# Optimization experiments

Measured on AMD Instinct MI355X. Metric: run time of the kernel, lower is better.

The kernel has to match this reference:

```python
import jax, jax.numpy as jnp
import numpy as np

N_NODES = 50000
N_EDGES = 800000
HIDDEN = 128
NUM_LAYERS = 3
NEG_SLOPE = 0.2  # PyG GATConv default leaky_relu slope


def setup_inputs() -> dict:
    key = jax.random.key(0)
    ks = jax.random.split(key, 10)
    d = HIDDEN
    glorot = 1.0 / np.sqrt(d)
    inp = {
        "x": jax.random.normal(ks[0], (N_NODES, d), dtype=jnp.float32),
        "edge_index": jax.random.randint(ks[1], (2, N_EDGES), 0, N_NODES, dtype=jnp.int32),
        "edge_mask": jax.random.uniform(ks[2], (N_EDGES,), dtype=jnp.float32),
        # GATConv params (heads=1)
        "W_gat": jax.random.normal(ks[3], (d, d), dtype=jnp.float32) * glorot,
        "a_src": jax.random.normal(ks[4], (d,), dtype=jnp.float32) * glorot,
        "a_dst": jax.random.normal(ks[5], (d,), dtype=jnp.float32) * glorot,
        "b_gat": jnp.zeros((d,), dtype=jnp.float32),
        # Stacked GCNConv params
        "W_gcn": jax.random.normal(ks[6], (NUM_LAYERS, d, d), dtype=jnp.float32) * glorot,
        "b_gcn": jnp.zeros((NUM_LAYERS, d), dtype=jnp.float32),
    }
    return inp


def _seg_softmax(e, seg, n):
    m = jax.ops.segment_max(e, seg, num_segments=n)
    p = jnp.exp(e - m[seg])
    s = jax.ops.segment_sum(p, seg, num_segments=n)
    return p / s[seg]


def reference(x, edge_index, edge_mask, W_gat, a_src, a_dst, b_gat, W_gcn, b_gcn):
    N = x.shape[0]
    loops = jnp.arange(N, dtype=edge_index.dtype)
    src = jnp.concatenate([edge_index[0], loops])  # [E+N] with self loops
    dst = jnp.concatenate([edge_index[1], loops])

    # --- GATConv (heads=1, add_self_loops=True); edge_attr ignored (edge_dim=None) ---
    xp = x @ W_gat                                      # [N, d]
    e = jax.nn.leaky_relu((xp @ a_src)[src] + (xp @ a_dst)[dst], NEG_SLOPE)
    alpha = _seg_softmax(e, dst, N)                     # segment softmax over incoming edges
    h = jax.ops.segment_sum(alpha[:, None] * xp[src], dst, num_segments=N) + b_gat

    # --- GCN normalization with edge_mask as edge_weight (self-loop weight = 1) ---
    w = jnp.concatenate([edge_mask, jnp.ones((N,), dtype=edge_mask.dtype)])
    deg = jax.ops.segment_sum(w, dst, num_segments=N)
    dinv = jnp.where(deg > 0, jax.lax.rsqrt(jnp.maximum(deg, 1e-12)), 0.0)
    norm = dinv[src] * w * dinv[dst]                    # [E+N]

    outs = [h]
    for l in range(NUM_LAYERS):
        z = outs[-1] @ W_gcn[l]                         # [N, d]
        z = jax.ops.segment_sum(norm[:, None] * z[src], dst, num_segments=N) + b_gcn[l]
        outs.append(jax.nn.relu(z))

    # JumpingKnowledge 'max': elementwise max over layer outputs
    return jnp.max(jnp.stack(outs, axis=0), axis=0)
```

## Files before the change

kernel.cpp:

```cpp
#include <hip/hip_runtime.h>

#define HIDDEN 128
#define NEG_SLOPE 0.2f
#define P_SORT 256

typedef unsigned short ushort_t;
typedef __attribute__((ext_vector_type(8))) short short8;
typedef __attribute__((ext_vector_type(4))) float floatx4;

static inline size_t align_up(size_t x, size_t a){ return (x + a - 1) & ~(a - 1); }

__device__ __forceinline__ ushort_t f2b(float f){
  unsigned u = __float_as_uint(f);
  unsigned r = (u + 0x7FFFu + ((u >> 16) & 1u)) >> 16;
  return (ushort_t)r;
}

__device__ __forceinline__ float b2f(ushort_t u){
  return __uint_as_float(((unsigned)u) << 16);
}

__device__ __forceinline__ void fma8q(float* acc, uint2 v, float a){
  int x = (int)v.x, y = (int)v.y;
  acc[0] += a * (float)((x << 24) >> 24);
  acc[1] += a * (float)((x << 16) >> 24);
  acc[2] += a * (float)((x <<  8) >> 24);
  acc[3] += a * (float)( x        >> 24);
  acc[4] += a * (float)((y << 24) >> 24);
  acc[5] += a * (float)((y << 16) >> 24);
  acc[6] += a * (float)((y <<  8) >> 24);
  acc[7] += a * (float)( y        >> 24);
}

__device__ __forceinline__ uint2 packq8(const float* f, float qi){
  unsigned a = 0, b = 0;
  int q;
  q = (int)rintf(f[0]*qi); a |= ((unsigned)q & 255u);
  q = (int)rintf(f[1]*qi); a |= ((unsigned)q & 255u) << 8;
  q = (int)rintf(f[2]*qi); a |= ((unsigned)q & 255u) << 16;
  q = (int)rintf(f[3]*qi); a |= ((unsigned)q & 255u) << 24;
  q = (int)rintf(f[4]*qi); b |= ((unsigned)q & 255u);
  q = (int)rintf(f[5]*qi); b |= ((unsigned)q & 255u) << 8;
  q = (int)rintf(f[6]*qi); b |= ((unsigned)q & 255u) << 16;
  q = (int)rintf(f[7]*qi); b |= ((unsigned)q & 255u) << 24;
  uint2 r; r.x = a; r.y = b; return r;
}

__device__ __forceinline__ uint4 pack8(const float* f){
  uint4 u;
  u.x = (unsigned)f2b(f[0]) | ((unsigned)f2b(f[1]) << 16);
  u.y = (unsigned)f2b(f[2]) | ((unsigned)f2b(f[3]) << 16);
  u.z = (unsigned)f2b(f[4]) | ((unsigned)f2b(f[5]) << 16);
  u.w = (unsigned)f2b(f[6]) | ((unsigned)f2b(f[7]) << 16);
  return u;
}


__global__ __launch_bounds__(256) void k_b1cnt_cast(const int* __restrict__ dst,
                                                    int* __restrict__ bcnt,
                                                    const float* __restrict__ Wg,
                                                    const float* __restrict__ Wc,
                                                    ushort_t* __restrict__ Wt,
                                                    int E, int epb, int nbkt){
  int t = threadIdx.x;
  if (blockIdx.x >= P_SORT){
    int i = (blockIdx.x - P_SORT)*256 + t;
    int mat = i >> 14, idx = i & 16383;
    int k = idx >> 7, n = idx & 127;
    float v = (mat == 0) ? Wg[idx] : Wc[(mat-1)*16384 + idx];
    Wt[mat*16384 + n*128 + k] = f2b(v);
    return;
  }
  __shared__ unsigned c[256];
  c[t] = 0;
  __syncthreads();
  int e0 = blockIdx.x * epb;
  int e1 = min(E, e0 + epb);
  for (int e = e0 + t; e < e1; e += 256) atomicAdd(&c[dst[e] >> 8], 1u);
  __syncthreads();
  if (t < nbkt) bcnt[t * P_SORT + blockIdx.x] = (int)c[t];
}

__global__ void k_scan1(const int* __restrict__ in, int* __restrict__ incl,
                        int* __restrict__ blockSums, int M){
  __shared__ int sd[256];
  int t = threadIdx.x;
  int i = blockIdx.x*256 + t;
  int v = (i < M) ? in[i] : 0;
  sd[t] = v; __syncthreads();
  for (int off = 1; off < 256; off <<= 1){
    int add = (t >= off) ? sd[t-off] : 0;
    __syncthreads();
    sd[t] += add;
    __syncthreads();
  }
  if (i < M) incl[i] = sd[t];
  if (t == 255) blockSums[blockIdx.x] = sd[255];
}

__global__ void k_scan2(const int* __restrict__ blockSums, int* __restrict__ blockOffs, int nb){
  __shared__ int sd[256];
  __shared__ int carry;
  int t = threadIdx.x;
  if (t == 0) carry = 0;
  __syncthreads();
  for (int base = 0; base < nb; base += 256){
    int i = base + t;
    int v = (i < nb) ? blockSums[i] : 0;
    sd[t] = v; __syncthreads();
    for (int off = 1; off < 256; off <<= 1){
      int add = (t >= off) ? sd[t-off] : 0;
      __syncthreads();
      sd[t] += add;
      __syncthreads();
    }
    if (i < nb) blockOffs[i] = carry + sd[t] - v;
    __syncthreads();
    if (t == 0) carry += sd[255];
    __syncthreads();
  }
}

__global__ __launch_bounds__(256) void k_b1place(const int* __restrict__ src,
                                                 const int* __restrict__ dst,
                                                 const float* __restrict__ w,
                                                 const int* __restrict__ incl,
                                                 const int* __restrict__ bcnt,
                                                 const int* __restrict__ blockOffs,
                                                 int2* __restrict__ tpw,
                                                 int E, int epb, int nbkt){
  __shared__ int base_[256];
  __shared__ unsigned c[256];
  int t = threadIdx.x;
  c[t] = 0;
  if (t < nbkt){
    int idx = t * P_SORT + blockIdx.x;
    base_[t] = incl[idx] - bcnt[idx] + blockOffs[t];
  }
  __syncthreads();
  int e0 = blockIdx.x * epb;
  int e1 = min(E, e0 + epb);
  for (int e = e0 + t; e < e1; e += 256){
    int d = dst[e];
    int b = d >> 8;
    unsigned r = atomicAdd(&c[b], 1u);
    int pos = base_[b] + (int)r;
    tpw[pos] = make_int2((int)((unsigned)src[e] | ((unsigned)(d & 255) << 16)),
                         __float_as_int(w[e]));
  }
}

__global__ __launch_bounds__(256) void k_b2(const int2* __restrict__ tpw,
                                            const int* __restrict__ blockOffs,
                                            int2* __restrict__ col_sw,
                                            int* __restrict__ rowp,
                                            float* __restrict__ dinv,
                                            int N, int E, int nbkt){
  __shared__ int cnt[4096];
  __shared__ int tsum[256];
  __shared__ float wsum[256];
  int b = blockIdx.x, t = threadIdx.x;
  int e0 = blockOffs[b];
  int e1 = (b + 1 < nbkt) ? blockOffs[b + 1] : E;
  #pragma unroll
  for (int i = 0; i < 16; i++) cnt[t*16 + i] = 0;
  wsum[t] = 0.f;
  __syncthreads();
  for (int e = e0 + t; e < e1; e += 256){
    int2 pw = tpw[e];
    unsigned dl = ((unsigned)pw.x >> 16) & 255u;
    unsigned s  = ((unsigned)pw.x & 0xFFFFu) >> 12;
    atomicAdd(&cnt[(dl << 4) | s], 1);
  }
  __syncthreads();
  int loc[16]; int run = 0;
  #pragma unroll
  for (int i = 0; i < 16; i++){ loc[i] = run; run += cnt[t*16 + i]; }
  tsum[t] = run;
  __syncthreads();
  for (int off = 1; off < 256; off <<= 1){
    int add = (t >= off) ? tsum[t-off] : 0;
    __syncthreads();
    tsum[t] += add;
    __syncthreads();
  }
  int base = tsum[t] - run;
  #pragma unroll
  for (int i = 0; i < 16; i++) cnt[t*16 + i] = base + loc[i];
  int node = b*256 + t;
  if (node < N) rowp[node] = e0 + base;
  if (b == 0 && t == 0) rowp[N] = E;
  __syncthreads();
  for (int e = e0 + t; e < e1; e += 256){
    int2 pw = tpw[e];
    unsigned dl = ((unsigned)pw.x >> 16) & 255u;
    unsigned srcv = (unsigned)pw.x & 0xFFFFu;
    unsigned s = srcv >> 12;
    int pos = e0 + atomicAdd(&cnt[(dl << 4) | s], 1);
    col_sw[pos] = make_int2((int)srcv, pw.y);
    atomicAdd(&wsum[dl], __int_as_float(pw.y));
  }
  __syncthreads();
  if (node < N) dinv[node] = rsqrtf(wsum[t] + 1.0f);
}

__global__ __launch_bounds__(128) void k_gemm1(const float* __restrict__ Ain,
                                               const ushort_t* __restrict__ Wt,
                                               unsigned* __restrict__ zq,
                                               const float* __restrict__ a_src,
                                               const float* __restrict__ a_dst,
                                               const float* __restrict__ dinv,
                                               float4* __restrict__ attr4,
                                               float* __restrict__ sdst, int M){
  __shared__ uint4 zq8v[64][8];
  char (*zq8)[128] = (char(*)[128])zq8v;
  int wave = threadIdx.x >> 6, l = threadIdx.x & 63;
  int q = l >> 4, lm = l & 15;
  int rowBase = blockIdx.x*64 + wave*32;
  floatx4 acc[2][8];
  #pragma unroll
  for (int mt = 0; mt < 2; mt++)
    #pragma unroll
    for (int nt = 0; nt < 8; nt++) acc[mt][nt] = (floatx4){0.f,0.f,0.f,0.f};

  #pragma unroll
  for (int kc = 0; kc < 4; kc++){
    int k0 = kc*32 + q*8;
    short8 a[2];
    #pragma unroll
    for (int mt = 0; mt < 2; mt++){
      long r = rowBase + mt*16 + lm;
      if (r < M){
        const float* ap = Ain + r*128 + k0;
        float4 u = *(const float4*)ap;
        float4 v = *(const float4*)(ap + 4);
        short8 tv;
        tv[0]=(short)f2b(u.x); tv[1]=(short)f2b(u.y); tv[2]=(short)f2b(u.z); tv[3]=(short)f2b(u.w);
        tv[4]=(short)f2b(v.x); tv[5]=(short)f2b(v.y); tv[6]=(short)f2b(v.z); tv[7]=(short)f2b(v.w);
        a[mt] = tv;
      } else a[mt] = (short8){0,0,0,0,0,0,0,0};
    }
    #pragma unroll
    for (int nt = 0; nt < 8; nt++){
      short8 b = *(const short8*)(Wt + (nt*16 + lm)*128 + k0);
      acc[0][nt] = __builtin_amdgcn_mfma_f32_16x16x32_bf16(a[0], b, acc[0][nt], 0, 0, 0);
      acc[1][nt] = __builtin_amdgcn_mfma_f32_16x16x32_bf16(a[1], b, acc[1][nt], 0, 0, 0);
    }
  }
  float rms[2][4];
  #pragma unroll
  for (int mt = 0; mt < 2; mt++){
    #pragma unroll
    for (int r = 0; r < 4; r++){
      float rm = 0.f;
      #pragma unroll
      for (int nt = 0; nt < 8; nt++) rm = fmaxf(rm, fabsf(acc[mt][nt][r]));
      #pragma unroll
      for (int off = 1; off <= 8; off <<= 1) rm = fmaxf(rm, __shfl_xor(rm, off, 64));
      float qi = (rm > 0.f) ? 127.f/rm : 0.f;
      int lrow = wave*32 + mt*16 + q*4 + r;
      #pragma unroll
      for (int nt = 0; nt < 8; nt++)
        zq8[lrow][nt*16 + lm] = (char)(int)rintf(acc[mt][nt][r]*qi);
      rms[mt][r] = rm * (1.f/127.f);
    }
  }
  float as8[8], ad8[8];
  #pragma unroll
  for (int nt = 0; nt < 8; nt++){ as8[nt] = a_src[nt*16 + lm]; ad8[nt] = a_dst[nt*16 + lm]; }
  #pragma unroll
  for (int mt = 0; mt < 2; mt++){
    #pragma unroll
    for (int r = 0; r < 4; r++){
      float ps = 0.f, pd = 0.f;
      #pragma unroll
      for (int nt = 0; nt < 8; nt++){
        ps += acc[mt][nt][r] * as8[nt];
        pd += acc[mt][nt][r] * ad8[nt];
      }
      #pragma unroll
      for (int off = 1; off <= 8; off <<= 1){
        ps += __shfl_xor(ps, off, 64);
        pd += __shfl_xor(pd, off, 64);
      }
      long row = rowBase + mt*16 + q*4 + r;
      if (lm == 0 && row < M){
        attr4[row] = make_float4(ps, dinv[row], rms[mt][r], 0.f);
        sdst[row] = pd;
      }
    }
  }
  __syncthreads();
  {
    int t = threadIdx.x;
    int lrow = t >> 1, half = t & 1;
    long row = (long)blockIdx.x*64 + lrow;
    if (row < M){
      uint4* dq = (uint4*)zq + row*8 + half*4;
      #pragma unroll
      for (int k = 0; k < 4; k++) dq[k] = zq8v[lrow][half*4 + k];
    }
  }
}

__global__ __launch_bounds__(256) void k_agg0(const unsigned* __restrict__ zq,
                                              const int* __restrict__ rowp,
                                              const int2* __restrict__ col_sw,
                                              const float4* __restrict__ attr4,
                                              const float* __restrict__ sdst_,
                                              const float* __restrict__ bias,
                                              ushort_t* __restrict__ out,
                                              unsigned* __restrict__ g0,
                                              float* __restrict__ scd0, int N){
  int n = blockIdx.x*4 + (threadIdx.x >> 6);
  if (n >= N) return;
  int l = threadIdx.x & 63;
  int sub = l >> 4, q = l & 15;
  int rs = rowp[n], re = rowp[n+1];
  float4 an = attr4[n];
  float sdd = sdst_[n];
  float es = an.x + sdd;
  es = (es >= 0.f) ? es : NEG_SLOPE*es;
  float pself = __expf(es);

  const uint2* f8 = (const uint2*)zq;
  float acc[8] = {0.f,0.f,0.f,0.f,0.f,0.f,0.f,0.f};
  float ps = 0.f;
  int last = (re > rs) ? re - 1 : 0;
  for (int base = rs; base < re; base += 24){
    int2 p[6];
    #pragma unroll
    for (int j = 0; j < 6; j++){
      int e = base + sub + 4*j;
      p[j] = col_sw[min(e, last)];
    }
    float4 at[6];
    #pragma unroll
    for (int j = 0; j < 6; j++) at[j] = attr4[p[j].x];
    uint2 v[6];
    #pragma unroll
    for (int j = 0; j < 6; j++) v[j] = f8[(size_t)p[j].x*16 + q];
    #pragma unroll
    for (int j = 0; j < 6; j++){
      int e = base + sub + 4*j;
      float ee = at[j].x + sdd;
      ee = (ee >= 0.f) ? ee : NEG_SLOPE*ee;
      float pe = (e < re) ? __expf(ee) : 0.f;
      ps += pe;
      fma8q(acc, v[j], pe * at[j].z);
    }
  }
  ps += __shfl_xor(ps, 16, 64);
  ps += __shfl_xor(ps, 32, 64);
  float inv = 1.f / (ps + pself);
  #pragma unroll
  for (int j = 0; j < 8; j++){
    acc[j] += __shfl_xor(acc[j], 16, 64);
    acc[j] += __shfl_xor(acc[j], 32, 64);
  }
  if (sub == 0){
    #pragma unroll
    for (int j = 0; j < 8; j++) acc[j] *= inv;
    fma8q(acc, f8[(size_t)n*16 + q], pself * inv * an.z);
    float4 b0 = ((const float4*)bias)[q*2];
    float4 b1 = ((const float4*)bias)[q*2 + 1];
    acc[0]+=b0.x; acc[1]+=b0.y; acc[2]+=b0.z; acc[3]+=b0.w;
    acc[4]+=b1.x; acc[5]+=b1.y; acc[6]+=b1.z; acc[7]+=b1.w;
    ((uint4*)out)[(size_t)n*16 + q] = pack8(acc);
    float rm = 0.f;
    #pragma unroll
    for (int j = 0; j < 8; j++) rm = fmaxf(rm, fabsf(acc[j]));
    #pragma unroll
    for (int off = 1; off <= 8; off <<= 1) rm = fmaxf(rm, __shfl_xor(rm, off, 64));
    float qi = (rm > 0.f) ? 127.f/rm : 0.f;
    ((uint2*)g0)[(size_t)n*16 + q] = packq8(acc, qi);
    if (l == 0) scd0[n] = rm * (1.f/127.f) * an.y;
  }
}

__global__ __launch_bounds__(256) void k_ecoef(const int2* __restrict__ col_sw,
                                               const float* __restrict__ scd,
                                               int2* __restrict__ col_eq, int E){
  int e = blockIdx.x*256 + threadIdx.x;
  if (e < E){
    int2 sw = col_sw[e];
    col_eq[e] = make_int2(sw.x, __float_as_int(__int_as_float(sw.y) * scd[sw.x]));
  }
}

template<int MODE>
__global__ __launch_bounds__(256) void k_fagg(const unsigned* __restrict__ gin,
                                              const float* __restrict__ scd_prev,
                                              const int* __restrict__ rowp,
                                              const int2* __restrict__ col_eq,
                                              const float* __restrict__ dinv,
                                              const ushort_t* __restrict__ Wl,
                                              const float* __restrict__ bias,
                                              ushort_t* __restrict__ out,
                                              unsigned* __restrict__ gout,
                                              float* __restrict__ scd_out,
                                              const ushort_t* __restrict__ j0,
                                              const ushort_t* __restrict__ j1,
                                              const ushort_t* __restrict__ j2,
                                              float* __restrict__ yout, int N){
  __shared__ ushort_t At[16][136];
  __shared__ uint4 q8v[16][8];
  __shared__ unsigned rmaxs[16];
  char (*q8s)[128] = (char(*)[128])q8v;
  int wave = threadIdx.x >> 6, l = threadIdx.x & 63;
  int sub = l >> 4, q = l & 15;
  const uint2* f8 = (const uint2*)gin;
  int tile = blockIdx.x * 16;

  #pragma unroll
  for (int pair = 0; pair < 2; pair++){
    int rowA = wave*4 + pair*2, rowB = rowA + 1;
    int nA = tile + rowA, nB = tile + rowB;
    int rsA = 0, reA = 0, rsB = 0, reB = 0;
    float dnA = 0.f, spA = 0.f, dnB = 0.f, spB = 0.f;
    if (nA < N){ rsA = rowp[nA]; reA = rowp[nA+1]; dnA = dinv[nA]; spA = scd_prev[nA]; }
    if (nB < N){ rsB = rowp[nB]; reB = rowp[nB+1]; dnB = dinv[nB]; spB = scd_prev[nB]; }
    int lastA = (reA > rsA) ? reA - 1 : 0;
    int lastB = (reB > rsB) ? reB - 1 : 0;
    float accA[8] = {0.f,0.f,0.f,0.f,0.f,0.f,0.f,0.f};
    float accB[8] = {0.f,0.f,0.f,0.f,0.f,0.f,0.f,0.f};
    int baseA = rsA, baseB = rsB;
    while (baseA < reA || baseB < reB){
      int2 pA[6], pB[6];
      #pragma unroll
      for (int j = 0; j < 6; j++){
        int e = baseA + sub + 4*j;
        pA[j] = col_eq[min(e, lastA)];
      }
      #pragma unroll
      for (int j = 0; j < 6; j++){
        int e = baseB + sub + 4*j;
        pB[j] = col_eq[min(e, lastB)];
      }
      uint2 vA[6], vB[6];
      #pragma unroll
      for (int j = 0; j < 6; j++) vA[j] = f8[(size_t)pA[j].x*16 + q];
      #pragma unroll
      for (int j = 0; j < 6; j++) vB[j] = f8[(size_t)pB[j].x*16 + q];
      #pragma unroll
      for (int j = 0; j < 6; j++){
        int e = baseA + sub + 4*j;
        fma8q(accA, vA[j], (e < reA) ? __int_as_float(pA[j].y) : 0.f);
      }
      #pragma unroll
      for (int j = 0; j < 6; j++){
        int e = baseB + sub + 4*j;
        fma8q(accB, vB[j], (e < reB) ? __int_as_float(pB[j].y) : 0.f);
      }
      baseA += 24; baseB += 24;
    }
    #pragma unroll
    for (int j = 0; j < 8; j++){
      accA[j] += __shfl_xor(accA[j], 16, 64);
      accA[j] += __shfl_xor(accA[j], 32, 64);
      accB[j] += __shfl_xor(accB[j], 16, 64);
      accB[j] += __shfl_xor(accB[j], 32, 64);
    }
    if (sub == 0){
      if (nA < N) fma8q(accA, f8[(size_t)nA*16 + q], spA);
      #pragma unroll
      for (int j = 0; j < 8; j++) accA[j] *= dnA;
      *(uint4*)&At[rowA][q*8] = pack8(accA);
      if (nB < N) fma8q(accB, f8[(size_t)nB*16 + q], spB);
      #pragma unroll
      for (int j = 0; j < 8; j++) accB[j] *= dnB;
      *(uint4*)&At[rowB][q*8] = pack8(accB);
    }
  }
  if (threadIdx.x < 16) rmaxs[threadIdx.x] = 0u;
  __syncthreads();

  floatx4 co[2];
  co[0] = (floatx4){0.f,0.f,0.f,0.f};
  co[1] = (floatx4){0.f,0.f,0.f,0.f};
  #pragma unroll
  for (int kc = 0; kc < 4; kc++){
    int k0 = kc*32 + sub*8;
    short8 a = *(const short8*)&At[q][k0];
    #pragma unroll
    for (int ntl = 0; ntl < 2; ntl++){
      int nt = wave*2 + ntl;
      short8 b = *(const short8*)(Wl + (size_t)(nt*16 + q)*128 + k0);
      co[ntl] = __builtin_amdgcn_mfma_f32_16x16x32_bf16(a, b, co[ntl], 0, 0, 0);
    }
  }
  float vv[4][2];
  #pragma unroll
  for (int r = 0; r < 4; r++){
    int row = sub*4 + r;
    int node = tile + row;
    float lmax = 0.f;
    #pragma unroll
    for (int ntl = 0; ntl < 2; ntl++){
      int colg = wave*32 + ntl*16 + q;
      float v = co[ntl][r] + bias[colg];
      v = fmaxf(v, 0.f);
      vv[r][ntl] = v;
      lmax = fmaxf(lmax, v);
      if (node < N){
        size_t idx = (size_t)node*128 + colg;
        if (MODE == 1){
          out[idx] = f2b(v);
        } else {
          float m = fmaxf(fmaxf(b2f(j0[idx]), b2f(j1[idx])),
                          fmaxf(b2f(j2[idx]), v));
          yout[idx] = m;
        }
      }
    }
    if (MODE == 1) atomicMax(&rmaxs[row], __float_as_uint(lmax));
  }
  if (MODE == 1){
    __syncthreads();
    #pragma unroll
    for (int r = 0; r < 4; r++){
      int row = sub*4 + r;
      float rm = __uint_as_float(rmaxs[row]);
      float qi = (rm > 0.f) ? 127.f/rm : 0.f;
      #pragma unroll
      for (int ntl = 0; ntl < 2; ntl++){
        int colg = wave*32 + ntl*16 + q;
        q8s[row][colg] = (char)(int)rintf(vv[r][ntl]*qi);
      }
    }
    if (threadIdx.x < 16){
      int node = tile + threadIdx.x;
      if (node < N){
        float rm = __uint_as_float(rmaxs[threadIdx.x]);
        scd_out[node] = rm * (1.f/127.f) * dinv[node];
      }
    }
    __syncthreads();
    if (threadIdx.x < 128){
      int row = threadIdx.x >> 3, c = threadIdx.x & 7;
      int node = tile + row;
      if (node < N) ((uint4*)gout)[(size_t)node*8 + c] = q8v[row][c];
    }
  }
}

extern "C" void kernel_launch(void* const* d_in, const int* in_sizes, int n_in,
                              void* d_out, int out_size, void* d_ws, size_t ws_size,
                              hipStream_t stream){
  const float* x      = (const float*)d_in[0];
  const int*   eidx   = (const int*)d_in[1];
  const float* emask  = (const float*)d_in[2];
  const float* W_gat  = (const float*)d_in[3];
  const float* a_src  = (const float*)d_in[4];
  const float* a_dst  = (const float*)d_in[5];
  const float* b_gat  = (const float*)d_in[6];
  const float* W_gcn  = (const float*)d_in[7];
  const float* b_gcn  = (const float*)d_in[8];
  int N = in_sizes[0] / HIDDEN;
  int E = in_sizes[1] / 2;
  const int* src = eidx;
  const int* dst = eidx + E;

  char* p = (char*)d_ws;
  auto carve = [&](size_t bytes)->char*{ char* q = p; p += align_up(bytes, 512); return q; };
  ushort_t* h0   = (ushort_t*)carve((size_t)N*HIDDEN*2);
  ushort_t* h1   = (ushort_t*)carve((size_t)N*HIDDEN*2);
  ushort_t* h2   = (ushort_t*)carve((size_t)N*HIDDEN*2);
  ushort_t* Wt   = (ushort_t*)carve((size_t)4*HIDDEN*HIDDEN*2);
  unsigned* zq   = (unsigned*)carve((size_t)N*HIDDEN);
  unsigned* g0q  = (unsigned*)carve((size_t)N*HIDDEN);
  unsigned* g1q  = (unsigned*)carve((size_t)N*HIDDEN);
  unsigned* g2q  = (unsigned*)carve((size_t)N*HIDDEN);
  float* scd0    = (float*)carve((size_t)N*4);
  float* scd1    = (float*)carve((size_t)N*4);
  float* scd2    = (float*)carve((size_t)N*4);
  float4* attr4  = (float4*)carve((size_t)N*16);
  float* sdst    = (float*)carve((size_t)N*4);
  float* dinv    = (float*)carve((size_t)N*4);
  int*   rowp    = (int*)  carve((size_t)(N+1)*4);
  int2*  col_sw  = (int2*) carve((size_t)E*8);
  int2*  col_eq  = (int2*) carve((size_t)E*8);
  int2*  tpw     = (int2*) carve((size_t)E*8);
  int nbkt = (N + 255) >> 8;
  int M    = nbkt * P_SORT;
  int*   bcnt  = (int*)carve((size_t)M*4);
  int*   incl  = (int*)carve((size_t)M*4);
  int nbs = (M + 255) / 256;
  int*   blockSums = (int*)carve((size_t)nbs*4);
  int*   blockOffs = (int*)carve((size_t)nbs*4);
  (void)ws_size; (void)n_in; (void)out_size;

  int epb = (E + P_SORT - 1) / P_SORT;
  int gb  = (N + 63) / 64;
  int nwb = (N + 3) / 4;
  int nfb = (N + 15) / 16;
  int neb = (E + 255) / 256;

  k_b1cnt_cast<<<P_SORT + 256, 256, 0, stream>>>(dst, bcnt, W_gat, W_gcn, Wt, E, epb, nbkt);
  k_scan1  <<<nbs, 256, 0, stream>>>(bcnt, incl, blockSums, M);
  k_scan2  <<<1,   256, 0, stream>>>(blockSums, blockOffs, nbs);
  k_b1place<<<P_SORT, 256, 0, stream>>>(src, dst, emask, incl, bcnt, blockOffs,
                                        tpw, E, epb, nbkt);
  k_b2     <<<nbkt, 256, 0, stream>>>(tpw, blockOffs, col_sw, rowp, dinv, N, E, nbkt);

  k_gemm1<<<gb, 128, 0, stream>>>(x, Wt, zq, a_src, a_dst, dinv, attr4, sdst, N);

  k_agg0<<<nwb, 256, 0, stream>>>(zq, rowp, col_sw, attr4, sdst,
                                  b_gat, h0, g0q, scd0, N);

  k_ecoef<<<neb, 256, 0, stream>>>(col_sw, scd0, col_eq, E);
  k_fagg<1><<<nfb, 256, 0, stream>>>(g0q, scd0, rowp, col_eq, dinv,
                                     Wt + (size_t)1*16384, b_gcn + 0,
                                     h1, g1q, scd1,
                                     nullptr, nullptr, nullptr, nullptr, N);
  k_ecoef<<<neb, 256, 0, stream>>>(col_sw, scd1, col_eq, E);
  k_fagg<1><<<nfb, 256, 0, stream>>>(g1q, scd1, rowp, col_eq, dinv,
                                     Wt + (size_t)2*16384, b_gcn + 128,
                                     h2, g2q, scd2,
                                     nullptr, nullptr, nullptr, nullptr, N);
  k_ecoef<<<neb, 256, 0, stream>>>(col_sw, scd2, col_eq, E);
  k_fagg<2><<<nfb, 256, 0, stream>>>(g2q, scd2, rowp, col_eq, dinv,
                                     Wt + (size_t)3*16384, b_gcn + 256,
                                     nullptr, nullptr, nullptr,
                                     h0, h1, h2, (float*)d_out, N);
}
```

Before: 345.0 us.

## Fuse edge-coefficient scaling into aggregation and fold block-offset scan into consumers

The three k_ecoef launches are removed. Each k_fagg block now stages its tile's edge list into shared memory, scaling each edge weight by the source-node quantization scale; tiles with more than LCOL_CAP edges fall back to computing the scale inline. The aggregation loop goes from two interleaved rows per iteration to one row at a time. The single-block k_scan2 is also removed, and k_b1place and k_b2 each redo the small block-sum scan in shared memory. The aim is to save launches and the extra pass writing and reading col_eq, at the cost of less memory-level parallelism in the gather loop and some repeated scan work.

New measurement: 316.0 us, median of 2. -8.4%, faster.

```diff
diff --git a/kernel.cpp b/kernel.cpp
--- a/kernel.cpp
+++ b/kernel.cpp
@@ -3,6 +3,7 @@
 #define HIDDEN 128
 #define NEG_SLOPE 0.2f
 #define P_SORT 256
+#define LCOL_CAP 512
 
 typedef unsigned short ushort_t;
 typedef __attribute__((ext_vector_type(8))) short short8;
@@ -98,44 +99,31 @@
   if (t == 255) blockSums[blockIdx.x] = sd[255];
 }
 
-__global__ void k_scan2(const int* __restrict__ blockSums, int* __restrict__ blockOffs, int nb){
-  __shared__ int sd[256];
-  __shared__ int carry;
-  int t = threadIdx.x;
-  if (t == 0) carry = 0;
-  __syncthreads();
-  for (int base = 0; base < nb; base += 256){
-    int i = base + t;
-    int v = (i < nb) ? blockSums[i] : 0;
-    sd[t] = v; __syncthreads();
-    for (int off = 1; off < 256; off <<= 1){
-      int add = (t >= off) ? sd[t-off] : 0;
-      __syncthreads();
-      sd[t] += add;
-      __syncthreads();
-    }
-    if (i < nb) blockOffs[i] = carry + sd[t] - v;
-    __syncthreads();
-    if (t == 0) carry += sd[255];
-    __syncthreads();
-  }
-}
-
 __global__ __launch_bounds__(256) void k_b1place(const int* __restrict__ src,
                                                  const int* __restrict__ dst,
                                                  const float* __restrict__ w,
                                                  const int* __restrict__ incl,
                                                  const int* __restrict__ bcnt,
-                                                 const int* __restrict__ blockOffs,
+                                                 const int* __restrict__ blockSums,
                                                  int2* __restrict__ tpw,
                                                  int E, int epb, int nbkt){
   __shared__ int base_[256];
   __shared__ unsigned c[256];
+  __shared__ int sOf[256];
   int t = threadIdx.x;
   c[t] = 0;
+  int bs = (t < nbkt) ? blockSums[t] : 0;
+  sOf[t] = bs;
+  __syncthreads();
+  for (int off = 1; off < 256; off <<= 1){
+    int add = (t >= off) ? sOf[t-off] : 0;
+    __syncthreads();
+    sOf[t] += add;
+    __syncthreads();
+  }
   if (t < nbkt){
     int idx = t * P_SORT + blockIdx.x;
-    base_[t] = incl[idx] - bcnt[idx] + blockOffs[t];
+    base_[t] = incl[idx] - bcnt[idx] + (sOf[t] - bs);
   }
   __syncthreads();
   int e0 = blockIdx.x * epb;
@@ -151,7 +139,7 @@
 }
 
 __global__ __launch_bounds__(256) void k_b2(const int2* __restrict__ tpw,
-                                            const int* __restrict__ blockOffs,
+                                            const int* __restrict__ blockSums,
                                             int2* __restrict__ col_sw,
                                             int* __restrict__ rowp,
                                             float* __restrict__ dinv,
@@ -159,13 +147,21 @@
   __shared__ int cnt[4096];
   __shared__ int tsum[256];
   __shared__ float wsum[256];
+  __shared__ int sOf[256];
   int b = blockIdx.x, t = threadIdx.x;
-  int e0 = blockOffs[b];
-  int e1 = (b + 1 < nbkt) ? blockOffs[b + 1] : E;
   #pragma unroll
   for (int i = 0; i < 16; i++) cnt[t*16 + i] = 0;
   wsum[t] = 0.f;
-  __syncthreads();
+  sOf[t] = (t < nbkt) ? blockSums[t] : 0;
+  __syncthreads();
+  for (int off = 1; off < 256; off <<= 1){
+    int add = (t >= off) ? sOf[t-off] : 0;
+    __syncthreads();
+    sOf[t] += add;
+    __syncthreads();
+  }
+  int e1 = sOf[b];
+  int e0 = (b > 0) ? sOf[b-1] : 0;
   for (int e = e0 + t; e < e1; e += 256){
     int2 pw = tpw[e];
     unsigned dl = ((unsigned)pw.x >> 16) & 255u;
@@ -378,21 +374,11 @@
   }
 }
 
-__global__ __launch_bounds__(256) void k_ecoef(const int2* __restrict__ col_sw,
-                                               const float* __restrict__ scd,
-                                               int2* __restrict__ col_eq, int E){
-  int e = blockIdx.x*256 + threadIdx.x;
-  if (e < E){
-    int2 sw = col_sw[e];
-    col_eq[e] = make_int2(sw.x, __float_as_int(__int_as_float(sw.y) * scd[sw.x]));
-  }
-}
-
 template<int MODE>
 __global__ __launch_bounds__(256) void k_fagg(const unsigned* __restrict__ gin,
                                               const float* __restrict__ scd_prev,
                                               const int* __restrict__ rowp,
-                                              const int2* __restrict__ col_eq,
+                                              const int2* __restrict__ col_sw,
                                               const float* __restrict__ dinv,
                                               const ushort_t* __restrict__ Wl,
                                               const float* __restrict__ bias,
@@ -406,73 +392,81 @@
   __shared__ ushort_t At[16][136];
   __shared__ uint4 q8v[16][8];
   __shared__ unsigned rmaxs[16];
+  __shared__ int2 lcol[LCOL_CAP];
   char (*q8s)[128] = (char(*)[128])q8v;
   int wave = threadIdx.x >> 6, l = threadIdx.x & 63;
   int sub = l >> 4, q = l & 15;
   const uint2* f8 = (const uint2*)gin;
   int tile = blockIdx.x * 16;
 
-  #pragma unroll
-  for (int pair = 0; pair < 2; pair++){
-    int rowA = wave*4 + pair*2, rowB = rowA + 1;
-    int nA = tile + rowA, nB = tile + rowB;
-    int rsA = 0, reA = 0, rsB = 0, reB = 0;
-    float dnA = 0.f, spA = 0.f, dnB = 0.f, spB = 0.f;
-    if (nA < N){ rsA = rowp[nA]; reA = rowp[nA+1]; dnA = dinv[nA]; spA = scd_prev[nA]; }
-    if (nB < N){ rsB = rowp[nB]; reB = rowp[nB+1]; dnB = dinv[nB]; spB = scd_prev[nB]; }
-    int lastA = (reA > rsA) ? reA - 1 : 0;
-    int lastB = (reB > rsB) ? reB - 1 : 0;
-    float accA[8] = {0.f,0.f,0.f,0.f,0.f,0.f,0.f,0.f};
-    float accB[8] = {0.f,0.f,0.f,0.f,0.f,0.f,0.f,0.f};
-    int baseA = rsA, baseB = rsB;
-    while (baseA < reA || baseB < reB){
-      int2 pA[6], pB[6];
-      #pragma unroll
-      for (int j = 0; j < 6; j++){
-        int e = baseA + sub + 4*j;
-        pA[j] = col_eq[min(e, lastA)];
-      }
-      #pragma unroll
-      for (int j = 0; j < 6; j++){
-        int e = baseB + sub + 4*j;
-        pB[j] = col_eq[min(e, lastB)];
-      }
-      uint2 vA[6], vB[6];
-      #pragma unroll
-      for (int j = 0; j < 6; j++) vA[j] = f8[(size_t)pA[j].x*16 + q];
-      #pragma unroll
-      for (int j = 0; j < 6; j++) vB[j] = f8[(size_t)pB[j].x*16 + q];
-      #pragma unroll
-      for (int j = 0; j < 6; j++){
-        int e = baseA + sub + 4*j;
-        fma8q(accA, vA[j], (e < reA) ? __int_as_float(pA[j].y) : 0.f);
-      }
-      #pragma unroll
-      for (int j = 0; j < 6; j++){
-        int e = baseB + sub + 4*j;
-        fma8q(accB, vB[j], (e < reB) ? __int_as_float(pB[j].y) : 0.f);
-      }
-      baseA += 24; baseB += 24;
+  int E0 = rowp[tile];
+  int E1 = rowp[min(tile + 16, N)];
+  int ecnt = E1 - E0;
+  bool fast = (ecnt <= LCOL_CAP);
+  if (fast){
+    for (int i = threadIdx.x; i < ecnt; i += 256){
+      int2 sw = col_sw[E0 + i];
+      lcol[i] = make_int2(sw.x, __float_as_int(__int_as_float(sw.y) * scd_prev[sw.x]));
+    }
+  }
+  if (threadIdx.x < 16) rmaxs[threadIdx.x] = 0u;
+  __syncthreads();
+
+  for (int i = 0; i < 4; i++){
+    int row = wave*4 + i;
+    int n = tile + row;
+    int rs = 0, re = 0; float dn = 0.f, sprev = 0.f;
+    if (n < N){ rs = rowp[n]; re = rowp[n+1]; dn = dinv[n]; sprev = scd_prev[n]; }
+    int last = (re > rs) ? re - 1 : 0;
+    float acc[8] = {0.f,0.f,0.f,0.f,0.f,0.f,0.f,0.f};
+    if (fast){
+      for (int base = rs; base < re; base += 24){
+        int2 p[6];
+        #pragma unroll
+        for (int j = 0; j < 6; j++){
+          int e = base + sub + 4*j;
+          p[j] = lcol[min(e, last) - E0];
+        }
+        uint2 v[6];
+        #pragma unroll
+        for (int j = 0; j < 6; j++) v[j] = f8[(size_t)p[j].x*16 + q];
+        #pragma unroll
+        for (int j = 0; j < 6; j++){
+          int e = base + sub + 4*j;
+          fma8q(acc, v[j], (e < re) ? __int_as_float(p[j].y) : 0.f);
+        }
+      }
+    } else {
+      for (int base = rs; base < re; base += 24){
+        int2 p[6];
+        #pragma unroll
+        for (int j = 0; j < 6; j++){
+          int e = base + sub + 4*j;
+          int2 sw = col_sw[min(e, last)];
+          p[j] = make_int2(sw.x, __float_as_int(__int_as_float(sw.y) * scd_prev[sw.x]));
+        }
+        uint2 v[6];
+        #pragma unroll
+        for (int j = 0; j < 6; j++) v[j] = f8[(size_t)p[j].x*16 + q];
+        #pragma unroll
+        for (int j = 0; j < 6; j++){
+          int e = base + sub + 4*j;
+          fma8q(acc, v[j], (e < re) ? __int_as_float(p[j].y) : 0.f);
+        }
+      }
     }
     #pragma unroll
     for (int j = 0; j < 8; j++){
-      accA[j] += __shfl_xor(accA[j], 16, 64);
-      accA[j] += __shfl_xor(accA[j], 32, 64);
-      accB[j] += __shfl_xor(accB[j], 16, 64);
-      accB[j] += __shfl_xor(accB[j], 32, 64);
+      acc[j] += __shfl_xor(acc[j], 16, 64);
+      acc[j] += __shfl_xor(acc[j], 32, 64);
     }
     if (sub == 0){
-      if (nA < N) fma8q(accA, f8[(size_t)nA*16 + q], spA);
-      #pragma unroll
-      for (int j = 0; j < 8; j++) accA[j] *= dnA;
-      *(uint4*)&At[rowA][q*8] = pack8(accA);
-      if (nB < N) fma8q(accB, f8[(size_t)nB*16 + q], spB);
-      #pragma unroll
-      for (int j = 0; j < 8; j++) accB[j] *= dnB;
-      *(uint4*)&At[rowB][q*8] = pack8(accB);
-    }
-  }
-  if (threadIdx.x < 16) rmaxs[threadIdx.x] = 0u;
+      if (n < N) fma8q(acc, f8[(size_t)n*16 + q], sprev);
+      #pragma unroll
+      for (int j = 0; j < 8; j++) acc[j] *= dn;
+      *(uint4*)&At[row][q*8] = pack8(acc);
+    }
+  }
   __syncthreads();
 
   floatx4 co[2];
@@ -579,7 +573,6 @@
   float* dinv    = (float*)carve((size_t)N*4);
   int*   rowp    = (int*)  carve((size_t)(N+1)*4);
   int2*  col_sw  = (int2*) carve((size_t)E*8);
-  int2*  col_eq  = (int2*) carve((size_t)E*8);
   int2*  tpw     = (int2*) carve((size_t)E*8);
   int nbkt = (N + 255) >> 8;
   int M    = nbkt * P_SORT;
@@ -587,39 +580,33 @@
   int*   incl  = (int*)carve((size_t)M*4);
   int nbs = (M + 255) / 256;
   int*   blockSums = (int*)carve((size_t)nbs*4);
-  int*   blockOffs = (int*)carve((size_t)nbs*4);
   (void)ws_size; (void)n_in; (void)out_size;
 
   int epb = (E + P_SORT - 1) / P_SORT;
   int gb  = (N + 63) / 64;
   int nwb = (N + 3) / 4;
   int nfb = (N + 15) / 16;
-  int neb = (E + 255) / 256;
 
   k_b1cnt_cast<<<P_SORT + 256, 256, 0, stream>>>(dst, bcnt, W_gat, W_gcn, Wt, E, epb, nbkt);
   k_scan1  <<<nbs, 256, 0, stream>>>(bcnt, incl, blockSums, M);
-  k_scan2  <<<1,   256, 0, stream>>>(blockSums, blockOffs, nbs);
-  k_b1place<<<P_SORT, 256, 0, stream>>>(src, dst, emask, incl, bcnt, blockOffs,
+  k_b1place<<<P_SORT, 256, 0, stream>>>(src, dst, emask, incl, bcnt, blockSums,
                                         tpw, E, epb, nbkt);
-  k_b2     <<<nbkt, 256, 0, stream>>>(tpw, blockOffs, col_sw, rowp, dinv, N, E, nbkt);
+  k_b2     <<<nbkt, 256, 0, stream>>>(tpw, blockSums, col_sw, rowp, dinv, N, E, nbkt);
 
   k_gemm1<<<gb, 128, 0, stream>>>(x, Wt, zq, a_src, a_dst, dinv, attr4, sdst, N);
 
   k_agg0<<<nwb, 256, 0, stream>>>(zq, rowp, col_sw, attr4, sdst,
                                   b_gat, h0, g0q, scd0, N);
 
-  k_ecoef<<<neb, 256, 0, stream>>>(col_sw, scd0, col_eq, E);
-  k_fagg<1><<<nfb, 256, 0, stream>>>(g0q, scd0, rowp, col_eq, dinv,
+  k_fagg<1><<<nfb, 256, 0, stream>>>(g0q, scd0, rowp, col_sw, dinv,
                                      Wt + (size_t)1*16384, b_gcn + 0,
                                      h1, g1q, scd1,
                                      nullptr, nullptr, nullptr, nullptr, N);
-  k_ecoef<<<neb, 256, 0, stream>>>(col_sw, scd1, col_eq, E);
-  k_fagg<1><<<nfb, 256, 0, stream>>>(g1q, scd1, rowp, col_eq, dinv,
+  k_fagg<1><<<nfb, 256, 0, stream>>>(g1q, scd1, rowp, col_sw, dinv,
                                      Wt + (size_t)2*16384, b_gcn + 128,
                                      h2, g2q, scd2,
                                      nullptr, nullptr, nullptr, nullptr, N);
-  k_ecoef<<<neb, 256, 0, stream>>>(col_sw, scd2, col_eq, E);
-  k_fagg<2><<<nfb, 256, 0, stream>>>(g2q, scd2, rowp, col_eq, dinv,
+  k_fagg<2><<<nfb, 256, 0, stream>>>(g2q, scd2, rowp, col_sw, dinv,
                                      Wt + (size_t)3*16384, b_gcn + 256,
                                      nullptr, nullptr, nullptr,
                                      h0, h1, h2, (float*)d_out, N);
```
